# Optimization experiments

Hardware: AMD Instinct MI355X
Metric: run time of the kernel (lower is better)

The kernel has to match this reference:

```python
import jax, jax.numpy as jnp
import numpy as np

B = 20000       # batch (labeled) nodes
N1 = 80000      # first-order neighbor nodes
E = 800000      # edges in the sampled subgraph over B+N1 nodes
C_IN = 256
C_OUT = 256
NUM_D = 32
NB = C_IN // NUM_D   # 8 branches
NUM_M = 4096
NUM_N = 200000  # total graph nodes (c_indices buffer length)


def setup_inputs() -> dict:
    key = jax.random.key(0)
    ks = jax.random.split(key, 12)
    x = jax.random.normal(ks[0], (B, C_IN), dtype=jnp.float32)
    edge_index = jax.random.randint(ks[1], (2, E), 0, B + N1, dtype=jnp.int32)
    edge_weight = jax.random.uniform(ks[2], (E,), dtype=jnp.float32)
    c_indices = jax.random.randint(ks[3], (NB, NUM_N), 0, NUM_M, dtype=jnp.int32)
    first_order_idx = jax.random.randint(ks[4], (N1,), 0, NUM_N, dtype=jnp.int32)
    codebook = jax.random.normal(ks[5], (NB, NUM_M, 2 * NUM_D), dtype=jnp.float32)
    s = 1.0 / np.sqrt(C_IN)
    W_conv = jax.random.normal(ks[6], (C_IN, C_IN), dtype=jnp.float32) * s
    b_conv = jnp.zeros((C_IN,), dtype=jnp.float32)
    W_t = jax.random.normal(ks[7], (C_IN, C_OUT), dtype=jnp.float32) * s
    b_t = jnp.zeros((C_OUT,), dtype=jnp.float32)
    W_skip = jax.random.normal(ks[8], (C_IN, C_OUT), dtype=jnp.float32) * s
    b_skip = jnp.zeros((C_OUT,), dtype=jnp.float32)
    warm_up_rate = jnp.ones((1,), dtype=jnp.float32)
    return {
        'x': x, 'edge_weight': edge_weight, 'codebook': codebook,
        'W_conv': W_conv, 'b_conv': b_conv, 'W_t': W_t, 'b_t': b_t,
        'W_skip': W_skip, 'b_skip': b_skip, 'warm_up_rate': warm_up_rate,
        'c_indices': c_indices, 'first_order_idx': first_order_idx,
        'edge_index': edge_index,
    }


def reference(x, edge_weight, codebook, W_conv, b_conv, W_t, b_t,
              W_skip, b_skip, warm_up_rate, c_indices, first_order_idx,
              edge_index):
    nb = codebook.shape[0]
    D = codebook.shape[2] // 2
    n_total = x.shape[0] + first_order_idx.shape[0]

    # per-branch VQ codebook gather for first-order neighbors: [nb, N1, 2D]
    c_idx = c_indices[:, first_order_idx]                       # [nb, N1]
    cb = codebook[jnp.arange(nb)[:, None], c_idx]               # [nb, N1, 2D]
    # concat branches along feature dim -> [N1, nb*D]
    x_first_order = cb[:, :, :D].transpose(1, 0, 2).reshape(-1, nb * D)
    grad_first_order = cb[:, :, D:].transpose(1, 0, 2).reshape(-1, nb * D)

    # x_input = [batch rows; quantized neighbor rows]
    x_input = jnp.concatenate([x, x_first_order], axis=0)       # [B+N1, C]

    # GCN conv (normalize=False): aggregate (x@W) over weighted edges + bias
    xw = x_input @ W_conv                                       # [B+N1, C]
    msg = xw[edge_index[0]] * edge_weight[:, None]              # [E, C]
    x_output = jax.ops.segment_sum(msg, edge_index[1],
                                   num_segments=n_total) + b_conv

    # info_backward term (gradient pathway through quantized neighbors)
    info_backward = jnp.sum(x_output[x.shape[0]:] * grad_first_order) \
        * warm_up_rate[0]

    # output transform + skip connection on batch rows only
    out = x_output[:x.shape[0]] @ W_t + b_t + (x @ W_skip + b_skip)
    return out, info_backward
```

## Files before the change

kernel.cpp:

```cpp
#include <hip/hip_runtime.h>

#define B_NODES 20000
#define N1_NODES 80000
#define NTOT 100000
#define E_EDGES 800000
#define CIN 256
#define COUT 256
#define NUM_D 32
#define NB 8
#define NUM_M 4096
#define NUM_N 200000
#define NPART 2048
#define CAP 40
#define NXCVT 313
#define NG1 1563
#define EPB 512
#define NG2 626

typedef __attribute__((ext_vector_type(8))) short short8;
typedef __attribute__((ext_vector_type(8))) unsigned short ushort8;
typedef __attribute__((ext_vector_type(4))) float f32x4;

__device__ inline unsigned short f2bf(float f) {
    unsigned int u = __float_as_uint(f);
    u += 0x7FFFu + ((u >> 16) & 1u);
    return (unsigned short)(u >> 16);
}
__device__ inline float bf2f(unsigned short u) {
    return __uint_as_float((unsigned int)u << 16);
}

__device__ inline short8 pack2(float4 a, float4 b) {
    short8 r;
    r[0] = (short)f2bf(a.x); r[1] = (short)f2bf(a.y);
    r[2] = (short)f2bf(a.z); r[3] = (short)f2bf(a.w);
    r[4] = (short)f2bf(b.x); r[5] = (short)f2bf(b.y);
    r[6] = (short)f2bf(b.z); r[7] = (short)f2bf(b.w);
    return r;
}

__global__ __launch_bounds__(256) void prepw_kernel(
    const float* __restrict__ Wc, const float* __restrict__ Wt,
    const float* __restrict__ Ws, short* __restrict__ WcT,
    short* __restrict__ WoT, const float* __restrict__ x,
    unsigned short* __restrict__ xb)
{
    __shared__ float Ls[64][65];
    if (blockIdx.x < 48) {
        const int z   = blockIdx.x >> 4;
        const int rem = blockIdx.x & 15;
        const int kx  = rem & 3, ny = rem >> 2;
        const float* src = (z == 0) ? Wc : ((z == 1) ? Wt : Ws);
        short* dst = (z == 0) ? WcT : WoT;
        const int dstStride = (z == 0) ? 256 : 512;
        const int colOff = (z == 2) ? 256 : 0;

        const int k0 = kx * 64, n0 = ny * 64;
        const int tid = threadIdx.x;
        #pragma unroll
        for (int lp = 0; lp < 16; ++lp) {
            int idx = tid + lp * 256;
            int rr = idx >> 6, cc = idx & 63;
            Ls[rr][cc] = src[(size_t)(k0 + rr) * 256 + n0 + cc];
        }
        __syncthreads();
        #pragma unroll
        for (int lp = 0; lp < 16; ++lp) {
            int idx = tid + lp * 256;
            int rr = idx >> 6, cc = idx & 63;
            dst[(size_t)(n0 + rr) * dstStride + colOff + k0 + cc] =
                (short)f2bf(Ls[cc][rr]);
        }
    } else {
        const int base = (blockIdx.x - 48) * 256 + threadIdx.x;
        const int total8 = B_NODES * CIN / 8;
        for (int g = base; g < total8; g += NXCVT * 256) {
            const float4* src = (const float4*)(x + (size_t)g * 8);
            *(short8*)(xb + (size_t)g * 8) = pack2(src[0], src[1]);
        }
    }
}

__global__ __launch_bounds__(256) void gemm1_scat_kernel(
    const unsigned short* __restrict__ xb, const int* __restrict__ fo,
    const int* __restrict__ cind, const float* __restrict__ cb,
    const short* __restrict__ WcT, unsigned short* __restrict__ xwb,
    const int* __restrict__ ei, const float* __restrict__ ew,
    int* __restrict__ cnt, int2* __restrict__ esw)
{
    __shared__ short As[2][64 * 40];
    __shared__ short Bs[2][256 * 40];

    const int tid  = threadIdx.x;
    const int w    = tid >> 6, l = tid & 63;
    const int row0 = blockIdx.x * 64;
    const int r    = tid >> 2, q = tid & 3;
    const int grow = row0 + r;
    const int g16  = (l >> 4) * 8;

    f32x4 acc[4][4] = {};

    for (int kso = 0; kso < 4; ++kso) {
        #pragma unroll
        for (int h = 0; h < 2; ++h) {
            const int ks = kso * 2 + h;
            const int k0 = ks * 32;
            short8 sv = {0,0,0,0,0,0,0,0};
            if (grow < B_NODES) {
                sv = *(const short8*)(xb + (size_t)grow * CIN + k0 + q * 8);
            } else if (grow < NTOT) {
                int i = grow - B_NODES;
                int cidx = cind[ks * NUM_N + fo[i]];
                const float4* src = (const float4*)(cb +
                    ((size_t)(ks * NUM_M + cidx)) * (2 * NUM_D) + q * 8);
                sv = pack2(src[0], src[1]);
            }
            *(short8*)&As[h][r * 40 + q * 8] = sv;

            const short8* wp = (const short8*)(WcT + (size_t)tid * 256 + k0);
            short8* bd = (short8*)&Bs[h][tid * 40];
            bd[0] = wp[0]; bd[1] = wp[1]; bd[2] = wp[2]; bd[3] = wp[3];
        }
        __syncthreads();

        #pragma unroll
        for (int h = 0; h < 2; ++h) {
            short8 av[4], bv[4];
            #pragma unroll
            for (int m = 0; m < 4; ++m)
                av[m] = *(const short8*)&As[h][((l & 15) + 16 * m) * 40 + g16];
            #pragma unroll
            for (int n = 0; n < 4; ++n)
                bv[n] = *(const short8*)&Bs[h][((l & 15) + 16 * n + w * 64) * 40 + g16];
            #pragma unroll
            for (int m = 0; m < 4; ++m)
                #pragma unroll
                for (int n = 0; n < 4; ++n)
                    acc[m][n] = __builtin_amdgcn_mfma_f32_16x16x32_bf16(
                        av[m], bv[n], acc[m][n], 0, 0, 0);
        }
        __syncthreads();
    }

    #pragma unroll
    for (int m = 0; m < 4; ++m) {
        int rbase = row0 + 16 * m + (l >> 4) * 4;
        #pragma unroll
        for (int n = 0; n < 4; ++n) {
            int col = w * 64 + 16 * n + (l & 15);
            #pragma unroll
            for (int j = 0; j < 4; ++j) {
                int rr = rbase + j;
                if (rr < NTOT)
                    xwb[(size_t)rr * COUT + col] = f2bf(acc[m][n][j]);
            }
        }
    }

    const int ebase = blockIdx.x * EPB;
    #pragma unroll
    for (int it = 0; it < EPB / 256; ++it) {
        int e = ebase + it * 256 + tid;
        if (e < E_EDGES) {
            int dst = ei[E_EDGES + e];
            int pos = atomicAdd(&cnt[dst], 1);
            esw[(size_t)dst * CAP + pos] = make_int2(ei[e], __float_as_int(ew[e]));
        }
    }
}

__global__ __launch_bounds__(256) void gather_accum_kernel(
    const unsigned short* __restrict__ xwb, const int2* __restrict__ esw,
    const int* __restrict__ cnt, const float* __restrict__ b_conv,
    const int* __restrict__ fo, const int* __restrict__ cind,
    const float* __restrict__ cb,
    unsigned short* __restrict__ xoutb, float* __restrict__ scalpart)
{
    const int wid  = threadIdx.x >> 6;
    const int lane = threadIdx.x & 63;
    const int node = blockIdx.x * 4 + wid;
    if (node >= NTOT) return;

    const int half = lane >> 5;
    const int l32  = lane & 31;
    const int c0   = l32 * 8;

    float acc[8];
    if (half == 0) {
        float4 b0 = *(const float4*)(b_conv + c0);
        float4 b1 = *(const float4*)(b_conv + c0 + 4);
        acc[0] = b0.x; acc[1] = b0.y; acc[2] = b0.z; acc[3] = b0.w;
        acc[4] = b1.x; acc[5] = b1.y; acc[6] = b1.z; acc[7] = b1.w;
    } else {
        #pragma unroll
        for (int k = 0; k < 8; ++k) acc[k] = 0.0f;
    }

    const int s = node * CAP;
    const int e = s + cnt[node];
    for (int j = s; j < e; j += 8) {
        int2  p[4];
        float w[4];
        #pragma unroll
        for (int t = 0; t < 4; ++t) {
            int idx = j + 2 * t + half;
            bool valid = idx < e;
            p[t] = esw[valid ? idx : s];
            w[t] = valid ? __int_as_float(p[t].y) : 0.0f;
        }
        ushort8 u[4];
        #pragma unroll
        for (int t = 0; t < 4; ++t)
            u[t] = *(const ushort8*)(xwb + (size_t)p[t].x * CIN + c0);
        #pragma unroll
        for (int t = 0; t < 4; ++t) {
            #pragma unroll
            for (int k = 0; k < 8; ++k) acc[k] += bf2f(u[t][k]) * w[t];
        }
    }

    #pragma unroll
    for (int k = 0; k < 8; ++k) acc[k] += __shfl_xor(acc[k], 32, 64);

    if (node < B_NODES) {
        if (half == 0) {
            ushort8 o;
            #pragma unroll
            for (int k = 0; k < 8; ++k) o[k] = f2bf(acc[k]);
            *(ushort8*)(xoutb + (size_t)node * CIN + c0) = o;
        }
    } else {
        float v = 0.0f;
        if (half == 0) {
            int i = node - B_NODES;
            int b = l32 >> 2;
            int d = (l32 & 3) * 8;
            int cidx = cind[b * NUM_N + fo[i]];
            const float* gp = cb + ((size_t)(b * NUM_M + cidx)) * (2 * NUM_D)
                              + NUM_D + d;
            float4 g0 = *(const float4*)gp;
            float4 g1 = *(const float4*)(gp + 4);
            v = acc[0] * g0.x + acc[1] * g0.y + acc[2] * g0.z + acc[3] * g0.w
              + acc[4] * g1.x + acc[5] * g1.y + acc[6] * g1.z + acc[7] * g1.w;
        }
        #pragma unroll
        for (int off = 32; off > 0; off >>= 1) v += __shfl_down(v, off, 64);
        if (lane == 0)
            atomicAdd(&scalpart[node & (NPART - 1)], v);
    }
}

__global__ __launch_bounds__(256) void gemm2_fin_kernel(
    const unsigned short* __restrict__ xoutb, const unsigned short* __restrict__ xb,
    const short* __restrict__ WoT,
    const float* __restrict__ bt, const float* __restrict__ bskip,
    const float* __restrict__ scalpart, const float* __restrict__ wur,
    float* __restrict__ out)
{
    if (blockIdx.x == NG2) {
        __shared__ float wsum[4];
        float v = 0.0f;
        for (int i = threadIdx.x; i < NPART; i += 256) v += scalpart[i];
        #pragma unroll
        for (int off = 32; off > 0; off >>= 1) v += __shfl_down(v, off, 64);
        if ((threadIdx.x & 63) == 0) wsum[threadIdx.x >> 6] = v;
        __syncthreads();
        if (threadIdx.x == 0)
            out[(size_t)B_NODES * COUT] =
                (wsum[0] + wsum[1] + wsum[2] + wsum[3]) * wur[0];
        return;
    }

    __shared__ short As[2][64 * 40];
    __shared__ short Bs[2][128 * 40];
    __shared__ float bsum[128];

    const int tid  = threadIdx.x;
    const int w    = tid >> 6, l = tid & 63;
    const int row0 = (blockIdx.x >> 1) * 64;
    const int colbase = (blockIdx.x & 1) * 128;
    const int r    = tid >> 2, q = tid & 3;
    const int bc_  = tid >> 1, bq = tid & 1;
    const int grow = row0 + r;
    const int g16  = (l >> 4) * 8;

    if (tid < 128) bsum[tid] = bt[colbase + tid] + bskip[colbase + tid];

    f32x4 acc[4][2] = {};

    for (int kso = 0; kso < 8; ++kso) {
        #pragma unroll
        for (int h = 0; h < 2; ++h) {
            const int ks = kso * 2 + h;
            const int k0 = ks * 32;
            short8 sv = {0,0,0,0,0,0,0,0};
            if (grow < B_NODES) {
                const unsigned short* base = (ks < 8)
                    ? (xoutb + (size_t)grow * CIN + k0)
                    : (xb    + (size_t)grow * CIN + (k0 - 256));
                sv = *(const short8*)(base + q * 8);
            }
            *(short8*)&As[h][r * 40 + q * 8] = sv;

            const short8* wp = (const short8*)(WoT +
                (size_t)(colbase + bc_) * 512 + k0 + bq * 16);
            short8* bd = (short8*)&Bs[h][bc_ * 40 + bq * 16];
            bd[0] = wp[0]; bd[1] = wp[1];
        }
        __syncthreads();

        #pragma unroll
        for (int h = 0; h < 2; ++h) {
            short8 av[4], bv[2];
            #pragma unroll
            for (int m = 0; m < 4; ++m)
                av[m] = *(const short8*)&As[h][((l & 15) + 16 * m) * 40 + g16];
            #pragma unroll
            for (int n = 0; n < 2; ++n)
                bv[n] = *(const short8*)&Bs[h][((l & 15) + 16 * n + w * 32) * 40 + g16];
            #pragma unroll
            for (int m = 0; m < 4; ++m)
                #pragma unroll
                for (int n = 0; n < 2; ++n)
                    acc[m][n] = __builtin_amdgcn_mfma_f32_16x16x32_bf16(
                        av[m], bv[n], acc[m][n], 0, 0, 0);
        }
        __syncthreads();
    }

    #pragma unroll
    for (int m = 0; m < 4; ++m) {
        int rbase = row0 + 16 * m + (l >> 4) * 4;
        #pragma unroll
        for (int n = 0; n < 2; ++n) {
            int lcol = w * 32 + 16 * n + (l & 15);
            int col  = colbase + lcol;
            float bc = bsum[lcol];
            #pragma unroll
            for (int j = 0; j < 4; ++j) {
                int rr = rbase + j;
                if (rr < B_NODES)
                    out[(size_t)rr * COUT + col] = acc[m][n][j] + bc;
            }
        }
    }
}

extern "C" void kernel_launch(void* const* d_in, const int* in_sizes, int n_in,
                              void* d_out, int out_size, void* d_ws, size_t ws_size,
                              hipStream_t stream)
{
    const float* x       = (const float*)d_in[0];
    const float* ew      = (const float*)d_in[1];
    const float* cb      = (const float*)d_in[2];
    const float* W_conv  = (const float*)d_in[3];
    const float* b_conv  = (const float*)d_in[4];
    const float* W_t     = (const float*)d_in[5];
    const float* b_t     = (const float*)d_in[6];
    const float* W_skip  = (const float*)d_in[7];
    const float* b_skip  = (const float*)d_in[8];
    const float* wur     = (const float*)d_in[9];
    const int*   cind    = (const int*)d_in[10];
    const int*   fo      = (const int*)d_in[11];
    const int*   ei      = (const int*)d_in[12];

    float* out = (float*)d_out;

    unsigned short* xwb   = (unsigned short*)d_ws;
    unsigned short* xoutb = xwb + (size_t)NTOT * CIN;
    unsigned short* xb    = xoutb + (size_t)B_NODES * CIN;
    short* WcT      = (short*)(xb + (size_t)B_NODES * CIN);
    short* WoT      = WcT + 256 * 256;
    int2*  esw      = (int2*)(WoT + 256 * 512);
    int*   cnt      = (int*)(esw + (size_t)NTOT * CAP);
    float* scalpart = (float*)(cnt + NTOT);

    hipMemsetAsync(cnt, 0, sizeof(int) * (NTOT + NPART), stream);

    prepw_kernel<<<48 + NXCVT, 256, 0, stream>>>(
        W_conv, W_t, W_skip, WcT, WoT, x, xb);

    gemm1_scat_kernel<<<NG1, 256, 0, stream>>>(
        xb, fo, cind, cb, WcT, xwb, ei, ew, cnt, esw);

    gather_accum_kernel<<<NTOT / 4, 256, 0, stream>>>(
        xwb, esw, cnt, b_conv, fo, cind, cb, xoutb, scalpart);

    gemm2_fin_kernel<<<NG2 + 1, 256, 0, stream>>>(
        xoutb, xb, WoT, b_t, b_skip, scalpart, wur, out);
}
```

Before: 191.5 us.

## Fold counter memset into prep kernel and split GEMM1 columns across two blocks

Result: faster. 178.0 us (-7.0%).

```diff
diff --git a/kernel.cpp b/kernel.cpp
--- a/kernel.cpp
+++ b/kernel.cpp
@@ -13,13 +13,15 @@
 #define NPART 2048
 #define CAP 40
 #define NXCVT 313
-#define NG1 1563
-#define EPB 512
+#define NZERO 100
+#define NG1 3126
+#define EPB 256
 #define NG2 626
 
 typedef __attribute__((ext_vector_type(8))) short short8;
 typedef __attribute__((ext_vector_type(8))) unsigned short ushort8;
 typedef __attribute__((ext_vector_type(4))) float f32x4;
+typedef __attribute__((ext_vector_type(4))) int i32x4;
 
 __device__ inline unsigned short f2bf(float f) {
     unsigned int u = __float_as_uint(f);
@@ -43,7 +45,7 @@
     const float* __restrict__ Wc, const float* __restrict__ Wt,
     const float* __restrict__ Ws, short* __restrict__ WcT,
     short* __restrict__ WoT, const float* __restrict__ x,
-    unsigned short* __restrict__ xb)
+    unsigned short* __restrict__ xb, int* __restrict__ cnt)
 {
     __shared__ float Ls[64][65];
     if (blockIdx.x < 48) {
@@ -71,13 +73,19 @@
             dst[(size_t)(n0 + rr) * dstStride + colOff + k0 + cc] =
                 (short)f2bf(Ls[cc][rr]);
         }
-    } else {
+    } else if (blockIdx.x < 48 + NXCVT) {
         const int base = (blockIdx.x - 48) * 256 + threadIdx.x;
         const int total8 = B_NODES * CIN / 8;
         for (int g = base; g < total8; g += NXCVT * 256) {
             const float4* src = (const float4*)(x + (size_t)g * 8);
             *(short8*)(xb + (size_t)g * 8) = pack2(src[0], src[1]);
         }
+    } else {
+        const int base = (blockIdx.x - 48 - NXCVT) * 256 + threadIdx.x;
+        const int total4 = (NTOT + NPART) / 4;
+        i32x4 z = {0, 0, 0, 0};
+        for (int g = base; g < total4; g += NZERO * 256)
+            ((i32x4*)cnt)[g] = z;
     }
 }
 
@@ -89,16 +97,18 @@
     int* __restrict__ cnt, int2* __restrict__ esw)
 {
     __shared__ short As[2][64 * 40];
-    __shared__ short Bs[2][256 * 40];
+    __shared__ short Bs[2][128 * 40];
 
     const int tid  = threadIdx.x;
     const int w    = tid >> 6, l = tid & 63;
-    const int row0 = blockIdx.x * 64;
+    const int row0 = (blockIdx.x >> 1) * 64;
+    const int colbase = (blockIdx.x & 1) * 128;
     const int r    = tid >> 2, q = tid & 3;
+    const int bc_  = tid >> 1, bq = tid & 1;
     const int grow = row0 + r;
     const int g16  = (l >> 4) * 8;
 
-    f32x4 acc[4][4] = {};
+    f32x4 acc[4][2] = {};
 
     for (int kso = 0; kso < 4; ++kso) {
         #pragma unroll
@@ -117,25 +127,26 @@
             }
             *(short8*)&As[h][r * 40 + q * 8] = sv;
 
-            const short8* wp = (const short8*)(WcT + (size_t)tid * 256 + k0);
-            short8* bd = (short8*)&Bs[h][tid * 40];
-            bd[0] = wp[0]; bd[1] = wp[1]; bd[2] = wp[2]; bd[3] = wp[3];
+            const short8* wp = (const short8*)(WcT +
+                (size_t)(colbase + bc_) * 256 + k0 + bq * 16);
+            short8* bd = (short8*)&Bs[h][bc_ * 40 + bq * 16];
+            bd[0] = wp[0]; bd[1] = wp[1];
         }
         __syncthreads();
 
         #pragma unroll
         for (int h = 0; h < 2; ++h) {
-            short8 av[4], bv[4];
+            short8 av[4], bv[2];
             #pragma unroll
             for (int m = 0; m < 4; ++m)
                 av[m] = *(const short8*)&As[h][((l & 15) + 16 * m) * 40 + g16];
             #pragma unroll
-            for (int n = 0; n < 4; ++n)
-                bv[n] = *(const short8*)&Bs[h][((l & 15) + 16 * n + w * 64) * 40 + g16];
+            for (int n = 0; n < 2; ++n)
+                bv[n] = *(const short8*)&Bs[h][((l & 15) + 16 * n + w * 32) * 40 + g16];
             #pragma unroll
             for (int m = 0; m < 4; ++m)
                 #pragma unroll
-                for (int n = 0; n < 4; ++n)
+                for (int n = 0; n < 2; ++n)
                     acc[m][n] = __builtin_amdgcn_mfma_f32_16x16x32_bf16(
                         av[m], bv[n], acc[m][n], 0, 0, 0);
         }
@@ -146,8 +157,8 @@
     for (int m = 0; m < 4; ++m) {
         int rbase = row0 + 16 * m + (l >> 4) * 4;
         #pragma unroll
-        for (int n = 0; n < 4; ++n) {
-            int col = w * 64 + 16 * n + (l & 15);
+        for (int n = 0; n < 2; ++n) {
+            int col = colbase + w * 32 + 16 * n + (l & 15);
             #pragma unroll
             for (int j = 0; j < 4; ++j) {
                 int rr = rbase + j;
@@ -157,15 +168,11 @@
         }
     }
 
-    const int ebase = blockIdx.x * EPB;
-    #pragma unroll
-    for (int it = 0; it < EPB / 256; ++it) {
-        int e = ebase + it * 256 + tid;
-        if (e < E_EDGES) {
-            int dst = ei[E_EDGES + e];
-            int pos = atomicAdd(&cnt[dst], 1);
-            esw[(size_t)dst * CAP + pos] = make_int2(ei[e], __float_as_int(ew[e]));
-        }
+    int e = blockIdx.x * EPB + tid;
+    if (e < E_EDGES) {
+        int dst = ei[E_EDGES + e];
+        int pos = atomicAdd(&cnt[dst], 1);
+        esw[(size_t)dst * CAP + pos] = make_int2(ei[e], __float_as_int(ew[e]));
     }
 }
 
@@ -375,10 +382,8 @@
     int*   cnt      = (int*)(esw + (size_t)NTOT * CAP);
     float* scalpart = (float*)(cnt + NTOT);
 
-    hipMemsetAsync(cnt, 0, sizeof(int) * (NTOT + NPART), stream);
-
-    prepw_kernel<<<48 + NXCVT, 256, 0, stream>>>(
-        W_conv, W_t, W_skip, WcT, WoT, x, xb);
+    prepw_kernel<<<48 + NXCVT + NZERO, 256, 0, stream>>>(
+        W_conv, W_t, W_skip, WcT, WoT, x, xb, cnt);
 
     gemm1_scat_kernel<<<NG1, 256, 0, stream>>>(
         xb, fo, cind, cb, WcT, xwb, ei, ew, cnt, esw);
```
